# Kernel optimization log

Hardware: AMD Instinct MI355X
Metric: run time of the kernel (lower is better)

Reference implementation:

```python
import jax, jax.numpy as jnp
import numpy as np

B, S, H, NH = 2, 2048, 2048, 32
HD = H // NH  # 64

def _causal_mask(b, s, dtype=jnp.float32):
    neg = jnp.finfo(dtype).min
    m = jnp.where(jnp.tril(jnp.ones((s, s), dtype=bool)), 0.0, neg).astype(dtype)
    return jnp.broadcast_to(m[None, None], (b, 1, s, s))

def setup_inputs() -> dict:
    key = jax.random.key(0)
    k1, k2, k3, k4, k5 = jax.random.split(key, 5)
    scale = 1.0 / np.sqrt(H)
    return {
        "hidden_states": jax.random.normal(k1, (B, S, H), jnp.float32),
        "attention_mask": _causal_mask(B, S),
        "Wq": jax.random.normal(k2, (H, H), jnp.float32) * scale,
        "Wk": jax.random.normal(k3, (H, H), jnp.float32) * scale,
        "Wv": jax.random.normal(k4, (H, H), jnp.float32) * scale,
        "Wo": jax.random.normal(k5, (H, H), jnp.float32) * scale,
    }

def reference(hidden_states, attention_mask, Wq, Wk, Wv, Wo):
    b, s, _ = hidden_states.shape
    dt = hidden_states.dtype
    def proj(W):  # torch Linear: x @ W.T -> [b, nh, s, hd]
        return (hidden_states @ W.T).reshape(b, s, NH, HD).transpose(0, 2, 1, 3)
    q, k, v = proj(Wq), proj(Wk), proj(Wv)
    attn = jnp.einsum('bhqd,bhkd->bhqk', q, k) / np.sqrt(HD)
    attn = attn + attention_mask
    attn = jnp.maximum(attn, jnp.finfo(attn.dtype).min)
    attn = jax.nn.softmax(attn.astype(jnp.float32), axis=-1).astype(dt)
    out = jnp.einsum('bhqk,bhkd->bhqd', attn, v)
    out = out.transpose(0, 2, 1, 3).reshape(b, s, H)
    return out @ Wo.T
```

## Files before the change

### kernel.cpp

```cpp
#include <hip/hip_runtime.h>
#include <hip/hip_bf16.h>
#include <stdint.h>

#define S_LEN 2048
#define NHEAD 32
#define HDIM  64

using bf16x8 = __attribute__((ext_vector_type(8))) short;
using f32x4  = __attribute__((ext_vector_type(4))) float;
using f32x16 = __attribute__((ext_vector_type(16))) float;

__device__ __forceinline__ uint16_t f2bf(float f) {
  union { float f; uint32_t u; } c; c.f = f;
  uint32_t u = c.u;
  return (uint16_t)((u + 0x7FFFu + ((u >> 16) & 1u)) >> 16);
}

__device__ __forceinline__ void load_lds16(const void* g, void* l) {
  __builtin_amdgcn_global_load_lds(
      (const __attribute__((address_space(1))) void*)g,
      (__attribute__((address_space(3))) void*)l, 16, 0, 0);
}

__device__ __forceinline__ f32x16 mfma32(bf16x8 a, bf16x8 b, f32x16 c) {
  return __builtin_amdgcn_mfma_f32_32x32x16_bf16(a, b, c, 0, 0, 0);
}

__device__ __forceinline__ uint32_t cvtpk(float lo, float hi_) {
  uint32_t d;
  asm("v_cvt_pk_bf16_f32 %0, %1, %2" : "=v"(d) : "v"(lo), "v"(hi_));
  return d;
}
__device__ __forceinline__ void plswap(uint32_t& a, uint32_t& b) {
  asm volatile("v_permlane32_swap_b32 %0, %1" : "+v"(a), "+v"(b));
}
__device__ __forceinline__ float exp2_hw(float x) {
  float r;
  asm("v_exp_f32 %0, %1" : "=v"(r) : "v"(x));
  return r;
}

__global__ __launch_bounds__(256) void conv_batch(
    const float* __restrict__ X, const float* __restrict__ Wq,
    const float* __restrict__ Wk, const float* __restrict__ Wv,
    const float* __restrict__ Wo, uint16_t* __restrict__ Xbf,
    uint16_t* __restrict__ Wqk, uint16_t* __restrict__ Wvb,
    uint16_t* __restrict__ Wob) {
  int i = blockIdx.x * 256 + threadIdx.x;
  const float* src; uint16_t* dst; int o;
  if (i < 2097152)      { src = X;  dst = Xbf;           o = i; }
  else if (i < 3145728) { src = Wq; dst = Wqk;           o = i - 2097152; }
  else if (i < 4194304) { src = Wk; dst = Wqk + 4194304; o = i - 3145728; }
  else if (i < 5242880) { src = Wv; dst = Wvb;           o = i - 4194304; }
  else                  { src = Wo; dst = Wob;           o = i - 5242880; }
  float4 v = ((const float4*)src)[o];
  uint64_t packed = (uint64_t)f2bf(v.x) | ((uint64_t)f2bf(v.y) << 16) |
                    ((uint64_t)f2bf(v.z) << 32) | ((uint64_t)f2bf(v.w) << 48);
  ((uint64_t*)dst)[o] = packed;
}

__global__ __launch_bounds__(512, 2) void gemm_qk(
    const uint16_t* __restrict__ A, const uint16_t* __restrict__ Bw,
    uint16_t* __restrict__ Qo, uint16_t* __restrict__ Ko, float qscale) {
  extern __shared__ char smem[];
  const int t = threadIdx.x;
  const int lane = t & 63, w = t >> 6;
  const int lrow = lane & 15, lgrp = lane >> 4;
  const int wr = w >> 2, wc = w & 3;
  const int id = blockIdx.x;
  const int swz = (id & 7) * 32 + (id >> 3);
  const int bm = (swz & 15) * 256, bn = (swz >> 4) * 256;
  constexpr int NT = 2048 / 32;

  const f32x4 zero4 = {0.f, 0.f, 0.f, 0.f};
  f32x4 acc[8][4];
#pragma unroll
  for (int mi = 0; mi < 8; ++mi)
#pragma unroll
    for (int ni = 0; ni < 4; ++ni) acc[mi][ni] = zero4;

  auto stage_mat = [&](const uint16_t* __restrict__ G, int grow0,
                       char* ldsbase, int kt) {
#pragma unroll
    for (int j = 0; j < 2; ++j) {
      const int s = t + j * 512;
      const int row = s >> 2;
      const int sc = (s & 3) ^ ((row >> 1) & 3);
      load_lds16(G + (size_t)(grow0 + row) * 2048 + kt + sc * 8,
                 ldsbase + j * 8192 + w * 1024);
    }
  };
  auto lda = [&](const char* Ab, int mi) -> bf16x8 {
    const int row = wr * 128 + mi * 16 + lrow;
    return *(const bf16x8*)(Ab + row * 64 + ((lgrp ^ ((row >> 1) & 3)) << 4));
  };
  auto ldb = [&](const char* Bb, int ni) -> bf16x8 {
    const int row = wc * 64 + ni * 16 + lrow;
    return *(const bf16x8*)(Bb + row * 64 + ((lgrp ^ ((row >> 1) & 3)) << 4));
  };

  stage_mat(A, bm, smem, 0);
  stage_mat(Bw, bn, smem + 16384, 0);
  stage_mat(A, bm, smem + 32768, 32);
  stage_mat(Bw, bn, smem + 32768 + 16384, 32);

  for (int kt = 0; kt < NT; ++kt) {
    char* cur = smem + (kt % 3) * 32768;
    char* nx2 = smem + ((kt + 2) % 3) * 32768;
    if (kt < NT - 1) asm volatile("s_waitcnt vmcnt(4)" ::: "memory");
    else             asm volatile("s_waitcnt vmcnt(0)" ::: "memory");
    __builtin_amdgcn_s_barrier();

    bf16x8 aF[4], bF[4];
#pragma unroll
    for (int mi = 0; mi < 4; ++mi) aF[mi] = lda(cur, mi);
#pragma unroll
    for (int ni = 0; ni < 4; ++ni) bF[ni] = ldb(cur + 16384, ni);
    if (kt + 2 < NT) stage_mat(A, bm, nx2, (kt + 2) * 32);
    __builtin_amdgcn_s_barrier();
    asm volatile("s_waitcnt lgkmcnt(0)" ::: "memory");
    __builtin_amdgcn_sched_barrier(0);
    __builtin_amdgcn_s_setprio(1);
#pragma unroll
    for (int mi = 0; mi < 4; ++mi)
#pragma unroll
      for (int ni = 0; ni < 4; ++ni)
        acc[mi][ni] = __builtin_amdgcn_mfma_f32_16x16x32_bf16(
            aF[mi], bF[ni], acc[mi][ni], 0, 0, 0);
    __builtin_amdgcn_s_setprio(0);
    __builtin_amdgcn_s_barrier();

    bf16x8 aG[4];
#pragma unroll
    for (int mi = 0; mi < 4; ++mi) aG[mi] = lda(cur, 4 + mi);
    if (kt + 2 < NT) stage_mat(Bw, bn, nx2 + 16384, (kt + 2) * 32);
    __builtin_amdgcn_s_barrier();
    asm volatile("s_waitcnt lgkmcnt(0)" ::: "memory");
    __builtin_amdgcn_sched_barrier(0);
    __builtin_amdgcn_s_setprio(1);
#pragma unroll
    for (int mi = 0; mi < 4; ++mi)
#pragma unroll
      for (int ni = 0; ni < 4; ++ni)
        acc[4 + mi][ni] = __builtin_amdgcn_mfma_f32_16x16x32_bf16(
            aG[mi], bF[ni], acc[4 + mi][ni], 0, 0, 0);
    __builtin_amdgcn_s_setprio(0);
  }

  const bool isQ = (bn < 2048);
#pragma unroll
  for (int mi = 0; mi < 8; ++mi) {
#pragma unroll
    for (int ni = 0; ni < 4; ++ni) {
      const int n = bn + wc * 64 + ni * 16 + lrow;
      const int n2 = isQ ? n : (n - 2048);
      const int h = n2 >> 6, d = n2 & 63;
#pragma unroll
      for (int r = 0; r < 4; ++r) {
        const int m = bm + wr * 128 + mi * 16 + lgrp * 4 + r;
        const int b = m >> 11, s = m & 2047;
        const size_t off = (((size_t)(b * NHEAD + h) * S_LEN + s) * HDIM) + d;
        if (isQ) Qo[off] = f2bf(acc[mi][ni][r] * qscale);
        else     Ko[off] = f2bf(acc[mi][ni][r]);
      }
    }
  }
}

template<int MODE>
__global__ __launch_bounds__(256, 3) void gemm_nt(
    const uint16_t* __restrict__ A, const uint16_t* __restrict__ B,
    void* __restrict__ C, int M, int N, int K, float scale) {
  __shared__ __align__(16) char smem[3][16384];

  const int t = threadIdx.x;
  const int lane = t & 63, w = t >> 6;
  const int lrow = lane & 15, lgrp = lane >> 4;
  const int bm = blockIdx.y * 128, bn = blockIdx.x * 128;
  const int wm = (w >> 1) * 64, wn = (w & 1) * 64;
  const int NT = K / 32;

  const f32x4 zero4 = {0.f, 0.f, 0.f, 0.f};
  f32x4 acc[4][4];
#pragma unroll
  for (int mi = 0; mi < 4; ++mi)
#pragma unroll
    for (int ni = 0; ni < 4; ++ni) acc[mi][ni] = zero4;

  auto stage_mat = [&](const uint16_t* __restrict__ G, int grow0,
                       char* ldsbase, int kt) {
#pragma unroll
    for (int j = 0; j < 2; ++j) {
      const int s = t + j * 256;
      const int row = s >> 2;
      const int sc = (s & 3) ^ ((row >> 1) & 3);
      load_lds16(G + (size_t)(grow0 + row) * K + kt + sc * 8,
                 ldsbase + j * 4096 + w * 1024);
    }
  };
  auto ldf = [&](const char* Mb, int base, int i) -> bf16x8 {
    const int row = base + i * 16 + lrow;
    return *(const bf16x8*)(Mb + row * 64 + ((lgrp ^ ((row >> 1) & 3)) << 4));
  };

  stage_mat(A, bm, smem[0], 0);
  stage_mat(B, bn, smem[0] + 8192, 0);
  stage_mat(A, bm, smem[1], 32);
  stage_mat(B, bn, smem[1] + 8192, 32);

  for (int kt = 0; kt < NT; ++kt) {
    char* cur = smem[kt % 3];
    if (kt < NT - 1) asm volatile("s_waitcnt vmcnt(4)" ::: "memory");
    else             asm volatile("s_waitcnt vmcnt(0)" ::: "memory");
    __builtin_amdgcn_s_barrier();

    if (kt + 2 < NT) {
      char* nx2 = smem[(kt + 2) % 3];
      stage_mat(A, bm, nx2, (kt + 2) * 32);
      stage_mat(B, bn, nx2 + 8192, (kt + 2) * 32);
    }

    bf16x8 aF[4], bF[4];
#pragma unroll
    for (int mi = 0; mi < 4; ++mi) aF[mi] = ldf(cur, wm, mi);
#pragma unroll
    for (int ni = 0; ni < 4; ++ni) bF[ni] = ldf(cur + 8192, wn, ni);
#pragma unroll
    for (int mi = 0; mi < 4; ++mi)
#pragma unroll
      for (int ni = 0; ni < 4; ++ni)
        acc[mi][ni] = __builtin_amdgcn_mfma_f32_16x16x32_bf16(
            aF[mi], bF[ni], acc[mi][ni], 0, 0, 0);
  }

#pragma unroll
  for (int mi = 0; mi < 4; ++mi) {
#pragma unroll
    for (int ni = 0; ni < 4; ++ni) {
      const int n = bn + wn + ni * 16 + lrow;
#pragma unroll
      for (int r = 0; r < 4; ++r) {
        const int m = bm + wm + mi * 16 + lgrp * 4 + r;
        const float v = acc[mi][ni][r] * scale;
        if (MODE == 2) {
          ((float*)C)[(size_t)m * N + n] = v;
        } else {
          const int h = m >> 6, d = m & 63;
          const int b = n >> 11, s = n & 2047;
          ((uint16_t*)C)[(((size_t)(b * NHEAD + h) * HDIM + d) * S_LEN) + s] =
              f2bf(v);
        }
      }
    }
  }
}

__global__ __launch_bounds__(256, 2) void attn_kernel(
    const uint16_t* __restrict__ Q, const uint16_t* __restrict__ K,
    const uint16_t* __restrict__ Vt, uint16_t* __restrict__ O) {
  extern __shared__ __align__(16) char asmem[];
  const int t = threadIdx.x, lane = t & 63, w = t >> 6;
  const int qcol = lane & 31, hi = lane >> 5;
  const int id = blockIdx.x;
  const int bh = (id & 7) * 8 + ((id >> 3) & 7);
  const int p = id >> 6;
  const int b = bh >> 5, h = bh & 31;

  const uint16_t* Qbh = Q + (size_t)bh * S_LEN * HDIM;
  const uint16_t* Kbh = K + (size_t)bh * S_LEN * HDIM;
  const uint16_t* Vbh = Vt + (size_t)bh * HDIM * S_LEN;

  const int srow = lane >> 3;
  const int schunk = (lane & 7) ^ srow;

  const short one_bf = (short)0x3F80;
  const bf16x8 onesf = {one_bf, one_bf, one_bf, one_bf,
                        one_bf, one_bf, one_bf, one_bf};

  auto Kbuf = [&](int bi, int sub) -> char* {
    return asmem + (bi * 2 + sub) * 8192;
  };
  auto Vbuf = [&](int bi, int sub) -> char* {
    return asmem + 32768 + (bi * 2 + sub) * 8192;
  };

  auto stage = [&](int k0, int bi) {
#pragma unroll
    for (int sub = 0; sub < 2; ++sub) {
      const int kb = k0 + sub * 64;
#pragma unroll
      for (int j = 0; j < 2; ++j) {
        const int r = j * 32 + w * 8 + srow;
        load_lds16(Kbh + (size_t)(kb + r) * HDIM + schunk * 8,
                   Kbuf(bi, sub) + j * 4096 + w * 1024);
        load_lds16(Vbh + (size_t)r * S_LEN + kb + schunk * 8,
                   Vbuf(bi, sub) + j * 4096 + w * 1024);
      }
    }
  };

  const int rk0 = qcol, rk1 = 32 + qcol;
  const int x0 = qcol & 7;

  for (int pass = 0; pass < 2; ++pass) {
    const int jq = pass ? (15 - p) : p;
    const int qw = jq * 128 + w * 32;
    const int qg = qw + qcol;

    bf16x8 qB[4];
    {
      const uint16_t* qp = Qbh + (size_t)qg * HDIM + hi * 8;
#pragma unroll
      for (int j = 0; j < 4; ++j) qB[j] = *(const bf16x8*)(qp + 16 * j);
    }

    f32x16 oacc0, oacc1, oS;
#pragma unroll
    for (int r = 0; r < 16; ++r) { oacc0[r] = 0.f; oacc1[r] = 0.f; oS[r] = 0.f; }

    auto qk = [&](const char* Kc, f32x16& s0, f32x16& s1) {
#pragma unroll
      for (int r = 0; r < 16; ++r) { s0[r] = 0.f; s1[r] = 0.f; }
      __builtin_amdgcn_s_setprio(1);
#pragma unroll
      for (int j = 0; j < 4; ++j) {
        bf16x8 kf0 = *(const bf16x8*)(Kc + rk0 * 128 + (((2*j+hi) ^ x0) << 4));
        bf16x8 kf1 = *(const bf16x8*)(Kc + rk1 * 128 + (((2*j+hi) ^ x0) << 4));
        s0 = mfma32(kf0, qB[j], s0);
        s1 = mfma32(kf1, qB[j], s1);
      }
      __builtin_amdgcn_s_setprio(0);
    };
    auto smx = [&](int k0s, f32x16& s0, f32x16& s1) {
      if (k0s + 63 > qw) {
#pragma unroll
        for (int r = 0; r < 16; ++r) {
          const int krow = (r & 3) + 8 * (r >> 2) + 4 * hi;
          s0[r] = (k0s + krow <= qg) ? exp2_hw(s0[r]) : 0.f;
          s1[r] = (k0s + 32 + krow <= qg) ? exp2_hw(s1[r]) : 0.f;
        }
      } else {
#pragma unroll
        for (int r = 0; r < 16; ++r) {
          s0[r] = exp2_hw(s0[r]);
          s1[r] = exp2_hw(s1[r]);
        }
      }
    };
    auto repack = [&](const f32x16& s0, const f32x16& s1, bf16x8 (&paf)[4]) {
#pragma unroll
      for (int tt = 0; tt < 4; ++tt) {
        const int o = 8 * (tt & 1);
        uint32_t a0, a1, a2, a3;
        if (tt < 2) {
          a0 = cvtpk(s0[o + 0], s0[o + 1]);
          a1 = cvtpk(s0[o + 2], s0[o + 3]);
          a2 = cvtpk(s0[o + 4], s0[o + 5]);
          a3 = cvtpk(s0[o + 6], s0[o + 7]);
        } else {
          a0 = cvtpk(s1[o + 0], s1[o + 1]);
          a1 = cvtpk(s1[o + 2], s1[o + 3]);
          a2 = cvtpk(s1[o + 4], s1[o + 5]);
          a3 = cvtpk(s1[o + 6], s1[o + 7]);
        }
        plswap(a0, a2);
        plswap(a1, a3);
        union { uint32_t u[4]; bf16x8 v; } pk;
        pk.u[0] = a0; pk.u[1] = a1; pk.u[2] = a2; pk.u[3] = a3;
        paf[tt] = pk.v;
      }
    };
    auto pv = [&](const char* Vc, const bf16x8 (&paf)[4]) {
      __builtin_amdgcn_s_setprio(1);
#pragma unroll
      for (int tt = 0; tt < 4; ++tt) {
        const int c = 2 * tt + hi;
        bf16x8 v0f = *(const bf16x8*)(Vc + rk0 * 128 + ((c ^ x0) << 4));
        bf16x8 v1f = *(const bf16x8*)(Vc + rk1 * 128 + ((c ^ x0) << 4));
        oacc0 = mfma32(paf[tt], v0f, oacc0);
        oacc1 = mfma32(paf[tt], v1f, oacc1);
        oS = mfma32(paf[tt], onesf, oS);
      }
      __builtin_amdgcn_s_setprio(0);
    };

    const int nt = jq + 1;
    for (int kt = 0; kt < nt; ++kt) {
      const int cur = kt & 1;
      const int k0 = kt * 128;
      if (kt == 0) { __syncthreads(); stage(0, 0); }
      __syncthreads();
      if (kt + 1 < nt) stage((kt + 1) * 128, cur ^ 1);

      const bool a1 = (k0 + 64 <= qw + 31);
      f32x16 s0a, s1a, s0b, s1b;
      qk(Kbuf(cur, 0), s0a, s1a);
      if (a1) qk(Kbuf(cur, 1), s0b, s1b);
      smx(k0, s0a, s1a);
      bf16x8 paf[4];
      repack(s0a, s1a, paf);
      pv(Vbuf(cur, 0), paf);
      if (a1) {
        smx(k0 + 64, s0b, s1b);
        repack(s0b, s1b, paf);
        pv(Vbuf(cur, 1), paf);
      }
    }

#pragma unroll
    for (int r = 0; r < 16; ++r) {
      const int qrow = (r & 3) + 8 * (r >> 2) + 4 * hi;
      const float inv = 1.0f / oS[r];
      const size_t base = ((size_t)b * S_LEN + qw + qrow) * 2048 + h * 64;
      O[base + qcol] = f2bf(oacc0[r] * inv);
      O[base + 32 + qcol] = f2bf(oacc1[r] * inv);
    }
  }
}

extern "C" void kernel_launch(void* const* d_in, const int* in_sizes, int n_in,
                              void* d_out, int out_size, void* d_ws,
                              size_t ws_size, hipStream_t stream) {
  const float* X  = (const float*)d_in[0];
  const float* Wq = (const float*)d_in[2];
  const float* Wk = (const float*)d_in[3];
  const float* Wv = (const float*)d_in[4];
  const float* Wo = (const float*)d_in[5];
  float* out = (float*)d_out;

  char* ws = (char*)d_ws;
  uint16_t* Xbf = (uint16_t*)ws;
  uint16_t* Wqk = (uint16_t*)(ws + 16777216);
  uint16_t* Qb  = (uint16_t*)(ws + 33554432);
  uint16_t* Kb  = (uint16_t*)(ws + 50331648);
  uint16_t* Wsm = (uint16_t*)(ws + 67108864);
  uint16_t* Wob = (uint16_t*)(ws + 75497472);
  uint16_t* Vtb = Wqk;
  uint16_t* Ob  = Xbf;

  const float qscale = 0.125f * 1.4426950408889634f;

  hipFuncSetAttribute((const void*)gemm_qk,
                      hipFuncAttributeMaxDynamicSharedMemorySize, 98304);
  hipFuncSetAttribute((const void*)attn_kernel,
                      hipFuncAttributeMaxDynamicSharedMemorySize, 65536);

  conv_batch<<<24576, 256, 0, stream>>>(X, Wq, Wk, Wv, Wo, Xbf, Wqk, Wsm, Wob);
  gemm_qk<<<256, 512, 98304, stream>>>(Xbf, Wqk, Qb, Kb, qscale);
  gemm_nt<1><<<dim3(32, 16), 256, 0, stream>>>(Wsm, Xbf, Vtb, 2048, 4096, 2048, 1.0f);
  attn_kernel<<<512, 256, 65536, stream>>>(Qb, Kb, Vtb, Ob);
  gemm_nt<2><<<dim3(16, 32), 256, 0, stream>>>(Ob, Wob, out, 4096, 2048, 2048, 1.0f);
}
```

Before: 221.7 us.

## Double K-tile to 64 in QK projection GEMM with double-buffered quadrant pipeline

The fused Q/K projection GEMM now uses a K tile of 64 instead of 32. It swaps the triple-buffered 32-wide stages for two 64KB buffers holding 128-row halves of A and B, with an 8-way XOR swizzle. Each iteration runs four MFMA quadrant phases and interleaves the next tile's global-to-LDS loads between them, so there are fewer barriers and waits per unit of K. In exchange, prefetch depth drops from two tiles ahead to one, with a full vmcnt(0) wait each iteration, and LDS use rises to 128KB per block.

```diff
diff --git a/kernel.cpp b/kernel.cpp
--- a/kernel.cpp
+++ b/kernel.cpp
@@ -70,7 +70,7 @@
   const int id = blockIdx.x;
   const int swz = (id & 7) * 32 + (id >> 3);
   const int bm = (swz & 15) * 256, bn = (swz >> 4) * 256;
-  constexpr int NT = 2048 / 32;
+  constexpr int NT = 2048 / 64;
 
   const f32x4 zero4 = {0.f, 0.f, 0.f, 0.f};
   f32x4 acc[8][4];
@@ -79,71 +79,115 @@
 #pragma unroll
     for (int ni = 0; ni < 4; ++ni) acc[mi][ni] = zero4;
 
-  auto stage_mat = [&](const uint16_t* __restrict__ G, int grow0,
-                       char* ldsbase, int kt) {
+  auto stage_half = [&](const uint16_t* __restrict__ G, int grow0,
+                        char* dstHalf, int kt) {
 #pragma unroll
     for (int j = 0; j < 2; ++j) {
       const int s = t + j * 512;
-      const int row = s >> 2;
-      const int sc = (s & 3) ^ ((row >> 1) & 3);
-      load_lds16(G + (size_t)(grow0 + row) * 2048 + kt + sc * 8,
-                 ldsbase + j * 8192 + w * 1024);
-    }
-  };
-  auto lda = [&](const char* Ab, int mi) -> bf16x8 {
-    const int row = wr * 128 + mi * 16 + lrow;
-    return *(const bf16x8*)(Ab + row * 64 + ((lgrp ^ ((row >> 1) & 3)) << 4));
-  };
-  auto ldb = [&](const char* Bb, int ni) -> bf16x8 {
-    const int row = wc * 64 + ni * 16 + lrow;
-    return *(const bf16x8*)(Bb + row * 64 + ((lgrp ^ ((row >> 1) & 3)) << 4));
-  };
-
-  stage_mat(A, bm, smem, 0);
-  stage_mat(Bw, bn, smem + 16384, 0);
-  stage_mat(A, bm, smem + 32768, 32);
-  stage_mat(Bw, bn, smem + 32768 + 16384, 32);
+      const int lr = s >> 3;
+      const int sc = (s & 7) ^ (lr & 7);
+      load_lds16(G + (size_t)(grow0 + lr) * 2048 + kt * 64 + sc * 8,
+                 dstHalf + j * 8192 + w * 1024);
+    }
+  };
+  auto ldA = [&](const char* bufA, int mh, int mi2, int kk) -> bf16x8 {
+    const int lr = mh * 64 + mi2 * 16 + lrow;
+    const int c = kk * 4 + lgrp;
+    return *(const bf16x8*)(bufA + wr * 16384 + lr * 128 +
+                            ((c ^ (lr & 7)) << 4));
+  };
+  auto ldB = [&](const char* bufB, int nh, int ni2, int kk) -> bf16x8 {
+    const int lr = (wc & 1) * 64 + nh * 32 + ni2 * 16 + lrow;
+    const int c = kk * 4 + lgrp;
+    return *(const bf16x8*)(bufB + (wc >> 1) * 16384 + lr * 128 +
+                            ((c ^ (lr & 7)) << 4));
+  };
+
+  stage_half(A, bm, smem, 0);
+  stage_half(A, bm + 128, smem + 16384, 0);
+  stage_half(Bw, bn, smem + 32768, 0);
+  stage_half(Bw, bn + 128, smem + 49152, 0);
 
   for (int kt = 0; kt < NT; ++kt) {
-    char* cur = smem + (kt % 3) * 32768;
-    char* nx2 = smem + ((kt + 2) % 3) * 32768;
-    if (kt < NT - 1) asm volatile("s_waitcnt vmcnt(4)" ::: "memory");
-    else             asm volatile("s_waitcnt vmcnt(0)" ::: "memory");
+    char* bufc = smem + (kt & 1) * 65536;
+    char* bufn = smem + ((kt + 1) & 1) * 65536;
+    const char* Ac = bufc;
+    const char* Bc = bufc + 32768;
+    const bool pre = (kt + 1 < NT);
+
+    asm volatile("s_waitcnt vmcnt(0)" ::: "memory");
     __builtin_amdgcn_s_barrier();
 
-    bf16x8 aF[4], bF[4];
-#pragma unroll
-    for (int mi = 0; mi < 4; ++mi) aF[mi] = lda(cur, mi);
-#pragma unroll
-    for (int ni = 0; ni < 4; ++ni) bF[ni] = ldb(cur + 16384, ni);
-    if (kt + 2 < NT) stage_mat(A, bm, nx2, (kt + 2) * 32);
-    __builtin_amdgcn_s_barrier();
+    bf16x8 aF[4][2], b0[2][2], b1[2][2];
+
+#pragma unroll
+    for (int mi2 = 0; mi2 < 4; ++mi2)
+#pragma unroll
+      for (int kk = 0; kk < 2; ++kk) aF[mi2][kk] = ldA(Ac, 0, mi2, kk);
+#pragma unroll
+    for (int ni2 = 0; ni2 < 2; ++ni2)
+#pragma unroll
+      for (int kk = 0; kk < 2; ++kk) b0[ni2][kk] = ldB(Bc, 0, ni2, kk);
+    if (pre) stage_half(A, bm, bufn, kt + 1);
     asm volatile("s_waitcnt lgkmcnt(0)" ::: "memory");
     __builtin_amdgcn_sched_barrier(0);
     __builtin_amdgcn_s_setprio(1);
 #pragma unroll
-    for (int mi = 0; mi < 4; ++mi)
-#pragma unroll
-      for (int ni = 0; ni < 4; ++ni)
-        acc[mi][ni] = __builtin_amdgcn_mfma_f32_16x16x32_bf16(
-            aF[mi], bF[ni], acc[mi][ni], 0, 0, 0);
+    for (int mi2 = 0; mi2 < 4; ++mi2)
+#pragma unroll
+      for (int ni2 = 0; ni2 < 2; ++ni2)
+#pragma unroll
+        for (int kk = 0; kk < 2; ++kk)
+          acc[mi2][ni2] = __builtin_amdgcn_mfma_f32_16x16x32_bf16(
+              aF[mi2][kk], b0[ni2][kk], acc[mi2][ni2], 0, 0, 0);
     __builtin_amdgcn_s_setprio(0);
-    __builtin_amdgcn_s_barrier();
-
-    bf16x8 aG[4];
-#pragma unroll
-    for (int mi = 0; mi < 4; ++mi) aG[mi] = lda(cur, 4 + mi);
-    if (kt + 2 < NT) stage_mat(Bw, bn, nx2 + 16384, (kt + 2) * 32);
-    __builtin_amdgcn_s_barrier();
+
+#pragma unroll
+    for (int ni2 = 0; ni2 < 2; ++ni2)
+#pragma unroll
+      for (int kk = 0; kk < 2; ++kk) b1[ni2][kk] = ldB(Bc, 1, ni2, kk);
+    if (pre) stage_half(A, bm + 128, bufn + 16384, kt + 1);
     asm volatile("s_waitcnt lgkmcnt(0)" ::: "memory");
     __builtin_amdgcn_sched_barrier(0);
     __builtin_amdgcn_s_setprio(1);
 #pragma unroll
-    for (int mi = 0; mi < 4; ++mi)
-#pragma unroll
-      for (int ni = 0; ni < 4; ++ni)
-        acc[4 + mi][ni] = __builtin_amdgcn_mfma_f32_16x16x32_bf16(
-            aG[mi], bF[ni], acc[4 + mi][ni], 0, 0, 0);
+    for (int mi2 = 0; mi2 < 4; ++mi2)
+#pragma unroll
+      for (int ni2 = 0; ni2 < 2; ++ni2)
+#pragma unroll
+        for (int kk = 0; kk < 2; ++kk)
+          acc[mi2][2 + ni2] = __builtin_amdgcn_mfma_f32_16x16x32_bf16(
+              aF[mi2][kk], b1[ni2][kk], acc[mi2][2 + ni2], 0, 0, 0);
+    __builtin_amdgcn_s_setprio(0);
+
+#pragma unroll
+    for (int mi2 = 0; mi2 < 4; ++mi2)
+#pragma unroll
+      for (int kk = 0; kk < 2; ++kk) aF[mi2][kk] = ldA(Ac, 1, mi2, kk);
+    if (pre) stage_half(Bw, bn, bufn + 32768, kt + 1);
+    asm volatile("s_waitcnt lgkmcnt(0)" ::: "memory");
+    __builtin_amdgcn_sched_barrier(0);
+    __builtin_amdgcn_s_setprio(1);
+#pragma unroll
+    for (int mi2 = 0; mi2 < 4; ++mi2)
+#pragma unroll
+      for (int ni2 = 0; ni2 < 2; ++ni2)
+#pragma unroll
+        for (int kk = 0; kk < 2; ++kk)
+          acc[4 + mi2][2 + ni2] = __builtin_amdgcn_mfma_f32_16x16x32_bf16(
+              aF[mi2][kk], b1[ni2][kk], acc[4 + mi2][2 + ni2], 0, 0, 0);
+    __builtin_amdgcn_s_setprio(0);
+
+    if (pre) stage_half(Bw, bn + 128, bufn + 49152, kt + 1);
+    __builtin_amdgcn_s_setprio(1);
+#pragma unroll
+    for (int mi2 = 0; mi2 < 4; ++mi2)
+#pragma unroll
+      for (int ni2 = 0; ni2 < 2; ++ni2)
+#pragma unroll
+        for (int kk = 0; kk < 2; ++kk)
+          acc[4 + mi2][ni2] = __builtin_amdgcn_mfma_f32_16x16x32_bf16(
+              aF[mi2][kk], b0[ni2][kk], acc[4 + mi2][ni2], 0, 0, 0);
     __builtin_amdgcn_s_setprio(0);
   }
 
@@ -441,12 +485,12 @@
   const float qscale = 0.125f * 1.4426950408889634f;
 
   hipFuncSetAttribute((const void*)gemm_qk,
-                      hipFuncAttributeMaxDynamicSharedMemorySize, 98304);
+                      hipFuncAttributeMaxDynamicSharedMemorySize, 131072);
   hipFuncSetAttribute((const void*)attn_kernel,
                       hipFuncAttributeMaxDynamicSharedMemorySize, 65536);
 
   conv_batch<<<24576, 256, 0, stream>>>(X, Wq, Wk, Wv, Wo, Xbf, Wqk, Wsm, Wob);
-  gemm_qk<<<256, 512, 98304, stream>>>(Xbf, Wqk, Qb, Kb, qscale);
+  gemm_qk<<<256, 512, 131072, stream>>>(Xbf, Wqk, Qb, Kb, qscale);
   gemm_nt<1><<<dim3(32, 16), 256, 0, stream>>>(Wsm, Xbf, Vtb, 2048, 4096, 2048, 1.0f);
   attn_kernel<<<512, 256, 65536, stream>>>(Qb, Kb, Vtb, Ob);
   gemm_nt<2><<<dim3(16, 32), 256, 0, stream>>>(Ob, Wob, out, 4096, 2048, 2048, 1.0f);
```

Measured after the change: 215.5 us. -2.8%, faster.
